# Optimization experiments

Hardware: AMD Instinct MI355X
Metric: run time of the kernel (lower is better)

## Reference

```python
import jax, jax.numpy as jnp
import numpy as np
from jax import lax

TAU = 10.0
THR = 1.0
ALPHA = float(np.exp(-1.0 / TAU))  # leak factor exp(-dt/tau), dt=1


def conv2d(x, w, pad):
    # x: [N,C,H,W], w: [O,I,kh,kw]
    return lax.conv_general_dilated(
        x, w, window_strides=(1, 1), padding=[(pad, pad), (pad, pad)],
        dimension_numbers=('NCHW', 'OIHW', 'NCHW'))


def avgpool(x, k):
    n, c, h, w = x.shape
    return x.reshape(n, c, h // k, k, w // k, k).mean(axis=(3, 5))


def exp_leak(x):
    # x: [T, ...]; v[t] = alpha*v[t-1] + x[t]; outputs membrane each step
    def step(v, xt):
        v = ALPHA * v + xt
        return v, v
    _, y = lax.scan(step, jnp.zeros_like(x[0]), x)
    return y


def lif(x):
    # LIF with SingleSpike + MembraneSubtract reset (norm_input=False)
    def step(v, xt):
        v = ALPHA * v + xt
        s = (v >= THR).astype(v.dtype)
        return v - s * THR, s
    _, s = lax.scan(step, jnp.zeros_like(x[0]), x)
    return s


def forward(x, conv1_w, conv2_w, lin_w):
    B, T = x.shape[:2]
    h = avgpool(conv2d(x.reshape(B * T, 2, 32, 32), conv1_w, 2), 4)  # [BT,4,8,8]
    h = h.reshape(B, T, 4, 8, 8).swapaxes(0, 1)                       # [T,B,4,8,8]
    h = lif(exp_leak(h)).swapaxes(0, 1).reshape(B * T, 4, 8, 8)
    h = avgpool(conv2d(h, conv2_w, 1), 2)                             # [BT,8,4,4]
    h = h.reshape(B, T, 8, 4, 4).swapaxes(0, 1)                       # [T,B,8,4,4]
    h = lif(exp_leak(h)).swapaxes(0, 1).reshape(B, T, 8 * 4 * 4)      # [B,T,128]
    return jnp.einsum('btf,of->bto', h, lin_w)                        # [B,T,2]


def setup_inputs() -> dict:
    key = jax.random.key(0)
    k1, k2, k3, k4 = jax.random.split(key, 4)
    B, T = 128, 100
    x = jax.random.uniform(k1, (B, T, 2, 32, 32), dtype=jnp.float32)
    conv1_w = jax.random.normal(k2, (4, 2, 5, 5), dtype=jnp.float32) / np.sqrt(2 * 5 * 5)
    conv2_w = jax.random.normal(k3, (8, 4, 3, 3), dtype=jnp.float32) / np.sqrt(4 * 3 * 3)
    lin_w = jax.random.normal(k4, (2, 128), dtype=jnp.float32) / np.sqrt(128)
    return {'x': x, 'conv1_w': conv1_w, 'conv2_w': conv2_w, 'lin_w': lin_w}


def reference(x, conv1_w, conv2_w, lin_w):
    return forward(x, conv1_w, conv2_w, lin_w)
```

## Files before the change

### kernel.cpp

```cpp
#include <hip/hip_runtime.h>

#define ALPHA 0.90483741803595957f

__global__ void prep_weights(const float* __restrict__ w1, const float* __restrict__ w2,
                             float* __restrict__ w1e, float* __restrict__ w2e) {
    int idx = blockIdx.x * 256 + threadIdx.x;
    if (idx < 512) {
        int v = idx & 7, u = (idx >> 3) & 7, ch = (idx >> 6) & 1, oc = idx >> 7;
        float s = 0.f;
        for (int a = 0; a < 5; ++a) {
            int i = u - a; if (i < 0 || i > 3) continue;
            for (int b = 0; b < 5; ++b) {
                int j = v - b; if (j < 0 || j > 3) continue;
                s += w1[((oc * 2 + ch) * 5 + a) * 5 + b];
            }
        }
        w1e[idx] = s * (1.f / 16.f);
    } else if (idx < 1024) {
        int k = idx - 512;
        int v = k & 3, u = (k >> 2) & 3, ch = (k >> 4) & 3, oc = k >> 6;
        float s = 0.f;
        for (int a = 0; a < 3; ++a) {
            int i = u - a; if (i < 0 || i > 1) continue;
            for (int b = 0; b < 3; ++b) {
                int j = v - b; if (j < 0 || j > 1) continue;
                s += w2[((oc * 4 + ch) * 3 + a) * 3 + b];
            }
        }
        w2e[k] = s * 0.25f;
    }
}

__global__ __launch_bounds__(256) void conv1_pool(const float* __restrict__ x,
                                                  const float* __restrict__ w1e,
                                                  float* __restrict__ y1) {
    __shared__ __align__(16) float tile[4][2][36][36];
    int tid = threadIdx.x;

    float4* t4 = (float4*)&tile[0][0][0][0];
    #pragma unroll
    for (int k = 0; k < 11; ++k) {
        int i = tid + k * 256;
        if (i < 2592) t4[i] = make_float4(0.f, 0.f, 0.f, 0.f);
    }
    __syncthreads();

    int li = tid >> 6, pos = tid & 63;
    long gi = (long)blockIdx.x * 4 + li;
    const float* src = x + gi * 2048;
    #pragma unroll
    for (int k = 0; k < 8; ++k) {
        int e = k * 256 + pos * 4;
        float4 d = *(const float4*)(src + e);
        int ch = e >> 10, rem = e & 1023, r = rem >> 5, c = rem & 31;
        float* dst = &tile[li][ch][r + 2][c + 2];
        dst[0] = d.x; dst[1] = d.y; dst[2] = d.z; dst[3] = d.w;
    }
    __syncthreads();

    int p = pos >> 3, q = pos & 7;
    float acc0 = 0.f, acc1 = 0.f, acc2 = 0.f, acc3 = 0.f;
    #pragma unroll
    for (int ch = 0; ch < 2; ++ch) {
        #pragma unroll
        for (int r = 0; r < 8; ++r) {
            const float* row = &tile[li][ch][4 * p + r][4 * q];
            float4 a = *(const float4*)row;
            float4 b = *(const float4*)(row + 4);
            float in[8] = {a.x, a.y, a.z, a.w, b.x, b.y, b.z, b.w};
            #pragma unroll
            for (int c = 0; c < 8; ++c) {
                float xi = in[c];
                acc0 += w1e[((0 * 2 + ch) * 8 + r) * 8 + c] * xi;
                acc1 += w1e[((1 * 2 + ch) * 8 + r) * 8 + c] * xi;
                acc2 += w1e[((2 * 2 + ch) * 8 + r) * 8 + c] * xi;
                acc3 += w1e[((3 * 2 + ch) * 8 + r) * 8 + c] * xi;
            }
        }
    }
    float* dst = y1 + gi * 256 + pos;
    dst[0] = acc0; dst[64] = acc1; dst[128] = acc2; dst[192] = acc3;
}

#define READW(base, Q)                                                        \
    {                                                                         \
        _Pragma("unroll")                                                     \
        for (int rr = 0; rr < 4; ++rr) {                                      \
            _Pragma("unroll")                                                 \
            for (int cc = 0; cc < 4; ++cc) {                                  \
                float4 tq = *(const float4*)((base) + rr * 40 + cc * 4);      \
                int o = (rr * 4 + cc) * 4;                                    \
                Q[o + 0] = tq.x; Q[o + 1] = tq.y;                             \
                Q[o + 2] = tq.z; Q[o + 3] = tq.w;                             \
            }                                                                 \
        }                                                                     \
    }

#define SCAN1_WRITE(in0, in1, in2, in3, d0, d1)                               \
    {                                                                         \
        v10 = ALPHA * v10 + (in0); v20 = ALPHA * v20 + v10;                   \
        float s0 = (v20 >= 1.f) ? 1.f : 0.f; v20 -= s0;                       \
        v11 = ALPHA * v11 + (in1); v21 = ALPHA * v21 + v11;                   \
        float s1 = (v21 >= 1.f) ? 1.f : 0.f; v21 -= s1;                       \
        v12 = ALPHA * v12 + (in2); v22 = ALPHA * v22 + v12;                   \
        float s2 = (v22 >= 1.f) ? 1.f : 0.f; v22 -= s2;                       \
        v13 = ALPHA * v13 + (in3); v23 = ALPHA * v23 + v13;                   \
        float s3 = (v23 >= 1.f) ? 1.f : 0.f; v23 -= s3;                       \
        float4 sp = make_float4(s0, s1, s2, s3);                              \
        *(float4*)(d0) = sp;                                                  \
        *(float4*)(d1) = sp;                                                  \
    }

#define CONV_SCAN2_STORE(Q, t)                                                \
    {                                                                         \
        float acca = 0.f, accb = 0.f;                                         \
        _Pragma("unroll")                                                     \
        for (int ch = 0; ch < 4; ++ch) {                                      \
            _Pragma("unroll")                                                 \
            for (int rr = 0; rr < 4; ++rr) {                                  \
                _Pragma("unroll")                                             \
                for (int cc = 0; cc < 4; ++cc) {                              \
                    float xv = Q[(rr * 4 + cc) * 4 + ch];                     \
                    acca += wa[ch * 16 + rr * 4 + cc] * xv;                   \
                    accb += wb[ch * 16 + rr * 4 + cc] * xv;                   \
                }                                                             \
            }                                                                 \
        }                                                                     \
        w1a = ALPHA * w1a + acca; w2a = ALPHA * w2a + w1a;                    \
        float sa = (w2a >= 1.f) ? 1.f : 0.f; w2a -= sa;                       \
        w1b = ALPHA * w1b + accb; w2b = ALPHA * w2b + w1b;                    \
        float sb = (w2b >= 1.f) ? 1.f : 0.f; w2b -= sb;                       \
        dst[(t) * 128]      = sa;                                             \
        dst[(t) * 128 + 64] = sb;                                             \
    }

__global__ __launch_bounds__(64, 1) void fused_wave(const float* __restrict__ y1,
                                                    const float* __restrict__ w2e,
                                                    float* __restrict__ s2g) {
    __shared__ float tE[808];
    __shared__ float tO[808];
    int lane = threadIdx.x;
    int b = blockIdx.x;

    #pragma unroll
    for (int k = 0; k < 13; ++k) {
        int i = lane + k * 64;
        if (i < 808) { tE[i] = 0.f; tO[i] = 0.f; }
    }

    int r1 = lane >> 3, c1 = lane & 7;
    int posq = ((r1 + 1) * 10 + (c1 + 1)) * 4;
    float* wE0 = &tE[posq];
    float* wE1 = &tE[404 + posq];
    float* wO0 = &tO[posq];
    float* wO1 = &tO[404 + posq];

    int oc = lane >> 4, p = (lane >> 2) & 3, q = lane & 3;

    float wa[64], wb[64];
    #pragma unroll
    for (int k = 0; k < 16; ++k) {
        float4 ta = *(const float4*)(w2e + oc * 64 + k * 4);
        float4 tb = *(const float4*)(w2e + (oc + 4) * 64 + k * 4);
        wa[k * 4 + 0] = ta.x; wa[k * 4 + 1] = ta.y; wa[k * 4 + 2] = ta.z; wa[k * 4 + 3] = ta.w;
        wb[k * 4 + 0] = tb.x; wb[k * 4 + 1] = tb.y; wb[k * 4 + 2] = tb.z; wb[k * 4 + 3] = tb.w;
    }

    int rbq = ((2 * p) * 10 + 2 * q) * 4 + ((p & 1) ? 404 : 0);
    const float* rbE = &tE[rbq];
    const float* rbO = &tO[rbq];

    #pragma unroll
    for (int k = 0; k < 64; ++k) {
        asm volatile("" : "+v"(wa[k]));
        asm volatile("" : "+v"(wb[k]));
    }

    const float* src = y1 + (long)b * 25600 + lane;
    float* dst = s2g + (long)b * 12800 + lane;

    float x0  = src[0],    x1  = src[64],   x2  = src[128],  x3  = src[192];
    float c10 = src[256],  c11 = src[320],  c12 = src[384],  c13 = src[448];
    float c20 = src[512],  c21 = src[576],  c22 = src[640],  c23 = src[704];
    float p10 = src[768],  p11 = src[832],  p12 = src[896],  p13 = src[960];
    float p20 = src[1024], p21 = src[1088], p22 = src[1152], p23 = src[1216];

    float v10 = 0.f, v20 = 0.f, v11 = 0.f, v21 = 0.f;
    float v12 = 0.f, v22 = 0.f, v13 = 0.f, v23 = 0.f;
    float w1a = 0.f, w2a = 0.f, w1b = 0.f, w2b = 0.f;

    float qa[64], qb[64];

    SCAN1_WRITE(x0, x1, x2, x3, wE0, wE1)
    READW(rbE, qa)

    for (int i = 0; i < 49; ++i) {
        int t5 = 2 * i + 5, t6 = 2 * i + 6;
        const float* a5 = src + (t5 < 100 ? t5 * 256 : 0);
        const float* a6 = src + (t6 < 100 ? t6 * 256 : 0);
        float n10 = a5[0], n11 = a5[64], n12 = a5[128], n13 = a5[192];
        float n20 = a6[0], n21 = a6[64], n22 = a6[128], n23 = a6[192];

        SCAN1_WRITE(c10, c11, c12, c13, wO0, wO1)
        READW(rbO, qb)
        CONV_SCAN2_STORE(qa, 2 * i)
        SCAN1_WRITE(c20, c21, c22, c23, wE0, wE1)
        READW(rbE, qa)
        CONV_SCAN2_STORE(qb, 2 * i + 1)

        c10 = p10; c11 = p11; c12 = p12; c13 = p13;
        c20 = p20; c21 = p21; c22 = p22; c23 = p23;
        p10 = n10; p11 = n11; p12 = n12; p13 = n13;
        p20 = n20; p21 = n21; p22 = n22; p23 = n23;
    }

    SCAN1_WRITE(c10, c11, c12, c13, wO0, wO1)
    READW(rbO, qb)
    CONV_SCAN2_STORE(qa, 98)
    CONV_SCAN2_STORE(qb, 99)
}

__global__ __launch_bounds__(256) void linear_out(const float* __restrict__ s2,
                                                  const float* __restrict__ lw,
                                                  float* __restrict__ out) {
    int tid = threadIdx.x;
    long bt = (long)blockIdx.x * 4 + (tid >> 6);
    int lane = tid & 63;
    float2 v = *(const float2*)(s2 + bt * 128 + lane * 2);
    float w00 = lw[lane * 2], w01 = lw[lane * 2 + 1];
    float w10 = lw[128 + lane * 2], w11 = lw[128 + lane * 2 + 1];
    float a0 = v.x * w00 + v.y * w01;
    float a1 = v.x * w10 + v.y * w11;
    #pragma unroll
    for (int off = 32; off; off >>= 1) {
        a0 += __shfl_down(a0, off);
        a1 += __shfl_down(a1, off);
    }
    if (lane == 0) { out[bt * 2] = a0; out[bt * 2 + 1] = a1; }
}

extern "C" void kernel_launch(void* const* d_in, const int* in_sizes, int n_in,
                              void* d_out, int out_size, void* d_ws, size_t ws_size,
                              hipStream_t stream) {
    const float* x  = (const float*)d_in[0];
    const float* w1 = (const float*)d_in[1];
    const float* w2 = (const float*)d_in[2];
    const float* lw = (const float*)d_in[3];
    float* out = (float*)d_out;

    float* ws   = (float*)d_ws;
    float* w1e  = ws;
    float* w2e  = ws + 512;
    float* y1   = ws + 1024;
    float* s2g  = y1 + 3276800;

    prep_weights<<<4, 256, 0, stream>>>(w1, w2, w1e, w2e);
    conv1_pool<<<3200, 256, 0, stream>>>(x, w1e, y1);
    fused_wave<<<128, 64, 0, stream>>>(y1, w2e, s2g);
    linear_out<<<3200, 256, 0, stream>>>(s2g, lw, out);
}
```

Measured before the change: 204.2 us.

## Process two batch samples per wave with interleaved independent scan chains

The fused scan/conv kernel now handles two batch elements per 64-thread block, interleaving their time steps so the two independent recurrences hide each other's latency, and launches 64 blocks instead of 128. Each sample uses its own LDS buffer rather than the even/odd double buffer of the single-sample version. This halves the number of waves on a GPU that was already underfilled. It also raises register pressure and lengthens the serial work per wave.

```diff
diff --git a/kernel.cpp b/kernel.cpp
--- a/kernel.cpp
+++ b/kernel.cpp
@@ -96,22 +96,22 @@
         }                                                                     \
     }
 
-#define SCAN1_WRITE(in0, in1, in2, in3, d0, d1)                               \
+#define SCAN1_W(V10,V20,V11,V21,V12,V22,V13,V23, I0,I1,I2,I3, D0,D1)          \
     {                                                                         \
-        v10 = ALPHA * v10 + (in0); v20 = ALPHA * v20 + v10;                   \
-        float s0 = (v20 >= 1.f) ? 1.f : 0.f; v20 -= s0;                       \
-        v11 = ALPHA * v11 + (in1); v21 = ALPHA * v21 + v11;                   \
-        float s1 = (v21 >= 1.f) ? 1.f : 0.f; v21 -= s1;                       \
-        v12 = ALPHA * v12 + (in2); v22 = ALPHA * v22 + v12;                   \
-        float s2 = (v22 >= 1.f) ? 1.f : 0.f; v22 -= s2;                       \
-        v13 = ALPHA * v13 + (in3); v23 = ALPHA * v23 + v13;                   \
-        float s3 = (v23 >= 1.f) ? 1.f : 0.f; v23 -= s3;                       \
+        V10 = ALPHA * V10 + (I0); V20 = ALPHA * V20 + V10;                    \
+        float s0 = (V20 >= 1.f) ? 1.f : 0.f; V20 -= s0;                       \
+        V11 = ALPHA * V11 + (I1); V21 = ALPHA * V21 + V11;                    \
+        float s1 = (V21 >= 1.f) ? 1.f : 0.f; V21 -= s1;                       \
+        V12 = ALPHA * V12 + (I2); V22 = ALPHA * V22 + V12;                    \
+        float s2 = (V22 >= 1.f) ? 1.f : 0.f; V22 -= s2;                       \
+        V13 = ALPHA * V13 + (I3); V23 = ALPHA * V23 + V13;                    \
+        float s3 = (V23 >= 1.f) ? 1.f : 0.f; V23 -= s3;                       \
         float4 sp = make_float4(s0, s1, s2, s3);                              \
-        *(float4*)(d0) = sp;                                                  \
-        *(float4*)(d1) = sp;                                                  \
-    }
-
-#define CONV_SCAN2_STORE(Q, t)                                                \
+        *(float4*)(D0) = sp;                                                  \
+        *(float4*)(D1) = sp;                                                  \
+    }
+
+#define CONV_S2_ST(Q, W1A,W2A,W1B,W2B, DST, T)                                \
     {                                                                         \
         float acca = 0.f, accb = 0.f;                                         \
         _Pragma("unroll")                                                     \
@@ -126,34 +126,34 @@
                 }                                                             \
             }                                                                 \
         }                                                                     \
-        w1a = ALPHA * w1a + acca; w2a = ALPHA * w2a + w1a;                    \
-        float sa = (w2a >= 1.f) ? 1.f : 0.f; w2a -= sa;                       \
-        w1b = ALPHA * w1b + accb; w2b = ALPHA * w2b + w1b;                    \
-        float sb = (w2b >= 1.f) ? 1.f : 0.f; w2b -= sb;                       \
-        dst[(t) * 128]      = sa;                                             \
-        dst[(t) * 128 + 64] = sb;                                             \
+        W1A = ALPHA * W1A + acca; W2A = ALPHA * W2A + W1A;                    \
+        float sa = (W2A >= 1.f) ? 1.f : 0.f; W2A -= sa;                       \
+        W1B = ALPHA * W1B + accb; W2B = ALPHA * W2B + W1B;                    \
+        float sb = (W2B >= 1.f) ? 1.f : 0.f; W2B -= sb;                       \
+        (DST)[(T) * 128]      = sa;                                           \
+        (DST)[(T) * 128 + 64] = sb;                                           \
     }
 
 __global__ __launch_bounds__(64, 1) void fused_wave(const float* __restrict__ y1,
                                                     const float* __restrict__ w2e,
                                                     float* __restrict__ s2g) {
-    __shared__ float tE[808];
-    __shared__ float tO[808];
+    __shared__ float T0[808];
+    __shared__ float T1[808];
     int lane = threadIdx.x;
-    int b = blockIdx.x;
+    long b0 = (long)blockIdx.x * 2;
 
     #pragma unroll
     for (int k = 0; k < 13; ++k) {
         int i = lane + k * 64;
-        if (i < 808) { tE[i] = 0.f; tO[i] = 0.f; }
+        if (i < 808) { T0[i] = 0.f; T1[i] = 0.f; }
     }
 
     int r1 = lane >> 3, c1 = lane & 7;
     int posq = ((r1 + 1) * 10 + (c1 + 1)) * 4;
-    float* wE0 = &tE[posq];
-    float* wE1 = &tE[404 + posq];
-    float* wO0 = &tO[posq];
-    float* wO1 = &tO[404 + posq];
+    float* wT0a = &T0[posq];
+    float* wT0b = &T0[404 + posq];
+    float* wT1a = &T1[posq];
+    float* wT1b = &T1[404 + posq];
 
     int oc = lane >> 4, p = (lane >> 2) & 3, q = lane & 3;
 
@@ -165,59 +165,81 @@
         wa[k * 4 + 0] = ta.x; wa[k * 4 + 1] = ta.y; wa[k * 4 + 2] = ta.z; wa[k * 4 + 3] = ta.w;
         wb[k * 4 + 0] = tb.x; wb[k * 4 + 1] = tb.y; wb[k * 4 + 2] = tb.z; wb[k * 4 + 3] = tb.w;
     }
-
-    int rbq = ((2 * p) * 10 + 2 * q) * 4 + ((p & 1) ? 404 : 0);
-    const float* rbE = &tE[rbq];
-    const float* rbO = &tO[rbq];
-
     #pragma unroll
     for (int k = 0; k < 64; ++k) {
         asm volatile("" : "+v"(wa[k]));
         asm volatile("" : "+v"(wb[k]));
     }
 
-    const float* src = y1 + (long)b * 25600 + lane;
-    float* dst = s2g + (long)b * 12800 + lane;
-
-    float x0  = src[0],    x1  = src[64],   x2  = src[128],  x3  = src[192];
-    float c10 = src[256],  c11 = src[320],  c12 = src[384],  c13 = src[448];
-    float c20 = src[512],  c21 = src[576],  c22 = src[640],  c23 = src[704];
-    float p10 = src[768],  p11 = src[832],  p12 = src[896],  p13 = src[960];
-    float p20 = src[1024], p21 = src[1088], p22 = src[1152], p23 = src[1216];
-
-    float v10 = 0.f, v20 = 0.f, v11 = 0.f, v21 = 0.f;
-    float v12 = 0.f, v22 = 0.f, v13 = 0.f, v23 = 0.f;
-    float w1a = 0.f, w2a = 0.f, w1b = 0.f, w2b = 0.f;
-
-    float qa[64], qb[64];
-
-    SCAN1_WRITE(x0, x1, x2, x3, wE0, wE1)
-    READW(rbE, qa)
-
-    for (int i = 0; i < 49; ++i) {
-        int t5 = 2 * i + 5, t6 = 2 * i + 6;
-        const float* a5 = src + (t5 < 100 ? t5 * 256 : 0);
-        const float* a6 = src + (t6 < 100 ? t6 * 256 : 0);
-        float n10 = a5[0], n11 = a5[64], n12 = a5[128], n13 = a5[192];
-        float n20 = a6[0], n21 = a6[64], n22 = a6[128], n23 = a6[192];
-
-        SCAN1_WRITE(c10, c11, c12, c13, wO0, wO1)
-        READW(rbO, qb)
-        CONV_SCAN2_STORE(qa, 2 * i)
-        SCAN1_WRITE(c20, c21, c22, c23, wE0, wE1)
-        READW(rbE, qa)
-        CONV_SCAN2_STORE(qb, 2 * i + 1)
-
-        c10 = p10; c11 = p11; c12 = p12; c13 = p13;
-        c20 = p20; c21 = p21; c22 = p22; c23 = p23;
-        p10 = n10; p11 = n11; p12 = n12; p13 = n13;
-        p20 = n20; p21 = n21; p22 = n22; p23 = n23;
-    }
-
-    SCAN1_WRITE(c10, c11, c12, c13, wO0, wO1)
-    READW(rbO, qb)
-    CONV_SCAN2_STORE(qa, 98)
-    CONV_SCAN2_STORE(qb, 99)
+    int rbq = ((2 * p) * 10 + 2 * q) * 4 + ((p & 1) ? 404 : 0);
+    const float* rb0 = &T0[rbq];
+    const float* rb1 = &T1[rbq];
+
+    const float* g0 = y1 + b0 * 25600 + lane;
+    const float* g1 = g0 + 25600;
+    float* d0 = s2g + b0 * 12800 + lane;
+    float* d1 = d0 + 12800;
+
+    __syncthreads();
+
+    float A10 = 0.f, A20 = 0.f, A11 = 0.f, A21 = 0.f,
+          A12 = 0.f, A22 = 0.f, A13 = 0.f, A23 = 0.f;
+    float B10 = 0.f, B20 = 0.f, B11 = 0.f, B21 = 0.f,
+          B12 = 0.f, B22 = 0.f, B13 = 0.f, B23 = 0.f;
+    float u1a = 0.f, u2a = 0.f, u1b = 0.f, u2b = 0.f;
+    float z1a = 0.f, z2a = 0.f, z1b = 0.f, z2b = 0.f;
+
+    float c0_0 = g0[0],    c0_1 = g0[64],   c0_2 = g0[128],  c0_3 = g0[192];
+    float c1_0 = g1[0],    c1_1 = g1[64],   c1_2 = g1[128],  c1_3 = g1[192];
+    float e0_0 = g0[256],  e0_1 = g0[320],  e0_2 = g0[384],  e0_3 = g0[448];
+    float e1_0 = g1[256],  e1_1 = g1[320],  e1_2 = g1[384],  e1_3 = g1[448];
+    float f0_0 = g0[512],  f0_1 = g0[576],  f0_2 = g0[640],  f0_3 = g0[704];
+    float f1_0 = g1[512],  f1_1 = g1[576],  f1_2 = g1[640],  f1_3 = g1[704];
+    float h0_0 = g0[768],  h0_1 = g0[832],  h0_2 = g0[896],  h0_3 = g0[960];
+    float h1_0 = g1[768],  h1_1 = g1[832],  h1_2 = g1[896],  h1_3 = g1[960];
+    float i0_0 = g0[1024], i0_1 = g0[1088], i0_2 = g0[1152], i0_3 = g0[1216];
+    float i1_0 = g1[1024], i1_1 = g1[1088], i1_2 = g1[1152], i1_3 = g1[1216];
+
+    float q0[64], q1[64];
+
+    SCAN1_W(A10,A20,A11,A21,A12,A22,A13,A23, c0_0,c0_1,c0_2,c0_3, wT0a,wT0b)
+    READW(rb0, q0)
+    SCAN1_W(B10,B20,B11,B21,B12,B22,B13,B23, c1_0,c1_1,c1_2,c1_3, wT1a,wT1b)
+    READW(rb1, q1)
+    CONV_S2_ST(q0, u1a,u2a,u1b,u2b, d0, 0)
+    c0_0=e0_0; c0_1=e0_1; c0_2=e0_2; c0_3=e0_3;
+    c1_0=e1_0; c1_1=e1_1; c1_2=e1_2; c1_3=e1_3;
+    e0_0=f0_0; e0_1=f0_1; e0_2=f0_2; e0_3=f0_3;
+    e1_0=f1_0; e1_1=f1_1; e1_2=f1_2; e1_3=f1_3;
+    f0_0=h0_0; f0_1=h0_1; f0_2=h0_2; f0_3=h0_3;
+    f1_0=h1_0; f1_1=h1_1; f1_2=h1_2; f1_3=h1_3;
+    h0_0=i0_0; h0_1=i0_1; h0_2=i0_2; h0_3=i0_3;
+    h1_0=i1_0; h1_1=i1_1; h1_2=i1_2; h1_3=i1_3;
+
+    for (int t = 1; t < 100; ++t) {
+        int tp = t + 4; const float* a0 = g0 + (tp < 100 ? tp * 256 : 0);
+        const float* a1 = g1 + (tp < 100 ? tp * 256 : 0);
+        float n0_0 = a0[0], n0_1 = a0[64], n0_2 = a0[128], n0_3 = a0[192];
+        float n1_0 = a1[0], n1_1 = a1[64], n1_2 = a1[128], n1_3 = a1[192];
+
+        SCAN1_W(A10,A20,A11,A21,A12,A22,A13,A23, c0_0,c0_1,c0_2,c0_3, wT0a,wT0b)
+        READW(rb0, q0)
+        CONV_S2_ST(q1, z1a,z2a,z1b,z2b, d1, t - 1)
+        SCAN1_W(B10,B20,B11,B21,B12,B22,B13,B23, c1_0,c1_1,c1_2,c1_3, wT1a,wT1b)
+        READW(rb1, q1)
+        CONV_S2_ST(q0, u1a,u2a,u1b,u2b, d0, t)
+
+        c0_0=e0_0; c0_1=e0_1; c0_2=e0_2; c0_3=e0_3;
+        c1_0=e1_0; c1_1=e1_1; c1_2=e1_2; c1_3=e1_3;
+        e0_0=f0_0; e0_1=f0_1; e0_2=f0_2; e0_3=f0_3;
+        e1_0=f1_0; e1_1=f1_1; e1_2=f1_2; e1_3=f1_3;
+        f0_0=h0_0; f0_1=h0_1; f0_2=h0_2; f0_3=h0_3;
+        f1_0=h1_0; f1_1=h1_1; f1_2=h1_2; f1_3=h1_3;
+        h0_0=n0_0; h0_1=n0_1; h0_2=n0_2; h0_3=n0_3;
+        h1_0=n1_0; h1_1=n1_1; h1_2=n1_2; h1_3=n1_3;
+    }
+
+    CONV_S2_ST(q1, z1a,z2a,z1b,z2b, d1, 99)
 }
 
 __global__ __launch_bounds__(256) void linear_out(const float* __restrict__ s2,
@@ -256,6 +278,6 @@
 
     prep_weights<<<4, 256, 0, stream>>>(w1, w2, w1e, w2e);
     conv1_pool<<<3200, 256, 0, stream>>>(x, w1e, y1);
-    fused_wave<<<128, 64, 0, stream>>>(y1, w2e, s2g);
+    fused_wave<<<64, 64, 0, stream>>>(y1, w2e, s2g);
     linear_out<<<3200, 256, 0, stream>>>(s2g, lw, out);
 }
```

After: 251.6 us. 23.2% more time.
